# Kernel tuning notes

Hardware: AMD Instinct MI355X
Metric: run time of the kernel (lower is better)

The kernel has to match this reference:

```python
import jax, jax.numpy as jnp
import numpy as np

N = 100000          # number of nodes
E = 128             # embedding size
NUM_LAYERS = 4
SMOOTH = 12.0       # MAXIMUM_SMOOTHNESS
RELATIONS = [("at", 2), ("clear", 1), ("on", 2)]  # sorted, as in module
ATOM_COUNTS = {"at": 150000, "clear": 150000, "on": 150000}


def mish(x):
    return x * jnp.tanh(jax.nn.softplus(x))


def _linear_init(k, din, dout):
    s = 1.0 / np.sqrt(din)
    kw, kb = jax.random.split(k)
    w = jax.random.uniform(kw, (din, dout), jnp.float32, -s, s)
    b = jax.random.uniform(kb, (dout,), jnp.float32, -s, s)
    return w, b


def setup_inputs() -> dict:
    key = jax.random.key(0)
    ks = iter(jax.random.split(key, 64))
    inp = {}
    inp["node_embeddings"] = jax.random.normal(next(ks), (N, E), jnp.float32)
    for name, ar in RELATIONS:
        inp[f"atoms_{name}"] = jax.random.randint(
            next(ks), (ATOM_COUNTS[name] * ar,), 0, N, dtype=jnp.int32)
        d = ar * E
        inp[f"w_in_{name}"], inp[f"b_in_{name}"] = _linear_init(next(ks), d, d)
        inp[f"w_out_{name}"], inp[f"b_out_{name}"] = _linear_init(next(ks), d, d)
    # update MLP: Linear(2E, 2E) -> mish -> Linear(2E, E)
    inp["w_u_in"], inp["b_u_in"] = _linear_init(next(ks), 2 * E, 2 * E)
    inp["w_u_out"], inp["b_u_out"] = _linear_init(next(ks), 2 * E, E)
    return inp


def _forward(node_embeddings, atoms, params):
    w_u_in, b_u_in, w_u_out, b_u_out = params["update"]

    def layer(h):
        msgs, idxs = [], []
        for name, ar in RELATIONS:
            w_in, b_in, w_out, b_out = params[name]
            av = atoms[name]                              # [A*ar] node indices
            x = h[av].reshape(-1, ar * E)                 # gather -> [A, ar*E]
            y = x + (mish(x @ w_in + b_in) @ w_out + b_out)  # residual MLP
            msgs.append(y.reshape(-1, E))
            idxs.append(av)
        msg = jnp.concatenate(msgs, 0)                    # [T, E]
        idx = jnp.concatenate(idxs, 0)                    # [T]
        # smooth-max aggregation (max offsets are not differentiated)
        seg_max = jax.ops.segment_max(msg, idx, num_segments=N)
        seg_max = jnp.where(jnp.isfinite(seg_max), seg_max, 0.0)  # empty -> 0 (include_self=False on zeros)
        seg_max = jax.lax.stop_gradient(seg_max)
        exps = jnp.exp(SMOOTH * (msg - seg_max[idx]))
        exps_sum = jax.ops.segment_sum(exps, idx, num_segments=N) + 1e-16
        max_msg = jnp.log(exps_sum) / SMOOTH + seg_max
        upd_in = jnp.concatenate([max_msg, h], axis=1)    # [N, 2E]
        upd = mish(upd_in @ w_u_in + b_u_in) @ w_u_out + b_u_out
        return h + upd                                    # outer residual

    h = node_embeddings
    for _ in range(NUM_LAYERS):
        h = layer(h)
    return h


def reference(node_embeddings, atoms_at, atoms_clear, atoms_on,
              w_in_at, b_in_at, w_out_at, b_out_at,
              w_in_clear, b_in_clear, w_out_clear, b_out_clear,
              w_in_on, b_in_on, w_out_on, b_out_on,
              w_u_in, b_u_in, w_u_out, b_u_out):
    atoms = {"at": atoms_at, "clear": atoms_clear, "on": atoms_on}
    params = {
        "at": (w_in_at, b_in_at, w_out_at, b_out_at),
        "clear": (w_in_clear, b_in_clear, w_out_clear, b_out_clear),
        "on": (w_in_on, b_in_on, w_out_on, b_out_on),
        "update": (w_u_in, b_u_in, w_u_out, b_u_out),
    }
    return _forward(node_embeddings, atoms, params)
```

## Files before the change

### kernel.cpp

```cpp
#include <hip/hip_runtime.h>
#include <hip/hip_bf16.h>
#include <math.h>

#define NNODES 100000
#define EDIM 128
#define TSLOTS 750000
#define NB 391

typedef __bf16 bf16x8 __attribute__((ext_vector_type(8)));
typedef __bf16 bf16x4 __attribute__((ext_vector_type(4)));
typedef float f32x4 __attribute__((ext_vector_type(4)));

#define T_SCALE 17.312340490667562f
#define INV_SCALE 0.05776226504666211f
#define EMPTY_V (-3.0701134f)

__device__ __forceinline__ float mishf(float x) {
  float u = __expf(fminf(x, 15.f));
  float num = u * (u + 2.f);
  return x * num * __builtin_amdgcn_rcpf(num + 2.f);
}

__device__ __forceinline__ double exp12t(float t) {
  t = fmaxf(t, -20000.f);
  float ti = floorf(t);
  float m = exp2f(t - ti);
  int ei = (int)ti;
  ei = ei < -1000 ? -1000 : (ei > 1000 ? 1000 : ei);
  return (double)m * __longlong_as_double(((long long)(1023 + ei)) << 52);
}

__device__ __forceinline__ float logS12(double S) {
  if (!(S > 0.0)) return EMPTY_V;
  long long b = __double_as_longlong(S);
  int e2 = (int)((b >> 52) & 0x7FF) - 1023;
  float mf = __uint_as_float(0x3F800000u | (unsigned)((b >> 29) & 0x7FFFFF));
  return ((float)e2 + log2f(mf)) * INV_SCALE;
}

__global__ void k_sentinel(float* out, int n) {
  int i = blockIdx.x * 256 + threadIdx.x;
  if (i < n) out[i] = 1.0e6f;
}

__global__ void k_init(const float* __restrict__ h0, __bf16* __restrict__ hb, int n8) {
  int i = blockIdx.x * 256 + threadIdx.x;
  if (i >= n8) return;
  float4 f0 = ((const float4*)h0)[i * 2];
  float4 f1 = ((const float4*)h0)[i * 2 + 1];
  bf16x8 p = {(__bf16)f0.x, (__bf16)f0.y, (__bf16)f0.z, (__bf16)f0.w,
              (__bf16)f1.x, (__bf16)f1.y, (__bf16)f1.z, (__bf16)f1.w};
  *(bf16x8*)(hb + (size_t)i * 8) = p;
}

struct TransDesc {
  const float* src[8];
  __bf16* dst[8];
  int R[8];
  int C[8];
  int tstart[9];
};

__global__ void k_transpose_all(TransDesc td) {
  __shared__ float tile[32][33];
  int b = blockIdx.x;
  int m = 0;
  while (m < 7 && b >= td.tstart[m + 1]) m++;
  int t = b - td.tstart[m];
  int R = td.R[m], C = td.C[m];
  int tcols = C >> 5;
  int by = t / tcols, bx = t - by * tcols;
  int tx = threadIdx.x & 31, ty = threadIdx.x >> 5;
  const float* src = td.src[m];
  __bf16* dst = td.dst[m];
  for (int i = 0; i < 32; i += 8)
    tile[ty + i][tx] = src[(size_t)(by * 32 + ty + i) * C + bx * 32 + tx];
  __syncthreads();
  for (int i = 0; i < 32; i += 8)
    dst[(size_t)(bx * 32 + ty + i) * R + by * 32 + tx] = (__bf16)tile[tx][ty + i];
}

__device__ __forceinline__ int slot_node(int s, const int* at, const int* cl, const int* on) {
  if (s < 300000) return at[s];
  if (s < 450000) return cl[s - 300000];
  return on[s - 450000];
}

__global__ void k_count(const int* __restrict__ at, const int* __restrict__ cl,
                        const int* __restrict__ on, int* __restrict__ cnt) {
  int s = blockIdx.x * 256 + threadIdx.x;
  if (s >= TSLOTS) return;
  atomicAdd(&cnt[slot_node(s, at, cl, on)], 1);
}

__global__ void k_bsum(const int* __restrict__ cnt, int* __restrict__ bsum) {
  __shared__ int sm[256];
  int n = blockIdx.x * 256 + threadIdx.x;
  sm[threadIdx.x] = (n < NNODES) ? cnt[n] : 0;
  __syncthreads();
  for (int st = 128; st > 0; st >>= 1) {
    if (threadIdx.x < st) sm[threadIdx.x] += sm[threadIdx.x + st];
    __syncthreads();
  }
  if (threadIdx.x == 0) bsum[blockIdx.x] = sm[0];
}

__global__ void k_bscan(const int* __restrict__ bsum, int* __restrict__ bpre,
                        int* __restrict__ off) {
  __shared__ int sm[512];
  int t = threadIdx.x;
  int v = (t < NB) ? bsum[t] : 0;
  sm[t] = v;
  __syncthreads();
  for (int st = 1; st < 512; st <<= 1) {
    int x = (t >= st) ? sm[t - st] : 0;
    __syncthreads();
    sm[t] += x;
    __syncthreads();
  }
  if (t < NB) bpre[t] = sm[t] - v;
  if (t == NB - 1) off[NNODES] = sm[t];
}

__global__ void k_off(const int* __restrict__ cnt, const int* __restrict__ bpre,
                      int* __restrict__ off) {
  __shared__ int sm[256];
  int n = blockIdx.x * 256 + threadIdx.x;
  int v = (n < NNODES) ? cnt[n] : 0;
  sm[threadIdx.x] = v;
  __syncthreads();
  for (int st = 1; st < 256; st <<= 1) {
    int t = (threadIdx.x >= st) ? sm[threadIdx.x - st] : 0;
    __syncthreads();
    sm[threadIdx.x] += t;
    __syncthreads();
  }
  if (n < NNODES) off[n] = bpre[blockIdx.x] + sm[threadIdx.x] - v;
}

__global__ void k_fill(const int* __restrict__ at, const int* __restrict__ cl,
                       const int* __restrict__ on, const int* __restrict__ off,
                       int* __restrict__ cnt, int* __restrict__ perm) {
  int s = blockIdx.x * 256 + threadIdx.x;
  if (s >= TSLOTS) return;
  int node = slot_node(s, at, cl, on);
  int pos = atomicAdd(&cnt[node], -1) - 1;
  perm[s] = off[node] + pos;
}

__global__ __launch_bounds__(256, 2) void k_rel2(
    const float* __restrict__ hf, const __bf16* __restrict__ hb,
    const int* __restrict__ av,
    const __bf16* __restrict__ wt1, const float* __restrict__ b1,
    const __bf16* __restrict__ wt2, const float* __restrict__ b2,
    _Float16* __restrict__ msg, const int* __restrict__ permrel, int A) {
  __shared__ __align__(16) __bf16 xs[64][264];
  __shared__ int avs[128];
  __shared__ int prm[128];
  const int tid = threadIdx.x;
  const int lane = tid & 63;
  const int w = tid >> 6;
  const int row0 = blockIdx.x * 64;

  if (tid < 128) {
    int i2 = row0 * 2 + tid;
    avs[tid] = (i2 < 2 * A) ? av[i2] : 0;
    prm[tid] = (i2 < 2 * A) ? permrel[i2] : 0;
  }
  if (hb != nullptr) {
    for (int i = 0; i < 8; ++i) {
      int s = tid + i * 256;
      int r = s >> 5, o = s & 31;
      int a = row0 + r;
      uint4 v = {0, 0, 0, 0};
      if (a < A) {
        int node = av[2 * a + (o >> 4)];
        v = *(const uint4*)(hb + (size_t)node * 128 + (o & 15) * 8);
      }
      *(uint4*)&xs[r][o * 8] = v;
    }
  } else {
    for (int i = 0; i < 16; ++i) {
      int s = tid + i * 256;
      int r = s >> 6, o = s & 63;
      int a = row0 + r;
      float4 f = {0.f, 0.f, 0.f, 0.f};
      if (a < A) {
        int node = av[2 * a + (o >> 5)];
        f = *(const float4*)(hf + (size_t)node * 128 + (o & 31) * 4);
      }
      bf16x4 p = {(__bf16)f.x, (__bf16)f.y, (__bf16)f.z, (__bf16)f.w};
      *(bf16x4*)&xs[r][o * 4] = p;
    }
  }
  __syncthreads();

  const int lhi = lane >> 4, llo = lane & 15;
  const int cb = w * 64;

  f32x4 acc1[4][4];
#pragma unroll
  for (int rt = 0; rt < 4; rt++)
#pragma unroll
    for (int ct = 0; ct < 4; ct++) acc1[rt][ct] = (f32x4){0.f, 0.f, 0.f, 0.f};

#pragma unroll
  for (int kk = 0; kk < 8; ++kk) {
    int k = kk * 32 + lhi * 8;
    bf16x8 af[4], bfr[4];
#pragma unroll
    for (int rt = 0; rt < 4; rt++) af[rt] = *(const bf16x8*)&xs[rt * 16 + llo][k];
#pragma unroll
    for (int ct = 0; ct < 4; ct++)
      bfr[ct] = *(const bf16x8*)(wt1 + (size_t)(cb + ct * 16 + llo) * 256 + k);
#pragma unroll
    for (int rt = 0; rt < 4; rt++)
#pragma unroll
      for (int ct = 0; ct < 4; ct++)
        acc1[rt][ct] = __builtin_amdgcn_mfma_f32_16x16x32_bf16(af[rt], bfr[ct], acc1[rt][ct], 0, 0, 0);
  }
  __syncthreads();

  float b1v[4];
#pragma unroll
  for (int ct = 0; ct < 4; ct++) b1v[ct] = b1[cb + ct * 16 + llo];
#pragma unroll
  for (int rt = 0; rt < 4; rt++)
#pragma unroll
    for (int ct = 0; ct < 4; ct++)
#pragma unroll
      for (int i = 0; i < 4; i++)
        xs[rt * 16 + lhi * 4 + i][cb + ct * 16 + llo] = (__bf16)mishf(acc1[rt][ct][i] + b1v[ct]);
  __syncthreads();

  f32x4 acc2[4][4];
#pragma unroll
  for (int rt = 0; rt < 4; rt++)
#pragma unroll
    for (int ct = 0; ct < 4; ct++) acc2[rt][ct] = (f32x4){0.f, 0.f, 0.f, 0.f};

#pragma unroll
  for (int kk = 0; kk < 8; ++kk) {
    int k = kk * 32 + lhi * 8;
    bf16x8 af[4], bfr[4];
#pragma unroll
    for (int rt = 0; rt < 4; rt++) af[rt] = *(const bf16x8*)&xs[rt * 16 + llo][k];
#pragma unroll
    for (int ct = 0; ct < 4; ct++)
      bfr[ct] = *(const bf16x8*)(wt2 + (size_t)(cb + ct * 16 + llo) * 256 + k);
#pragma unroll
    for (int rt = 0; rt < 4; rt++)
#pragma unroll
      for (int ct = 0; ct < 4; ct++)
        acc2[rt][ct] = __builtin_amdgcn_mfma_f32_16x16x32_bf16(af[rt], bfr[ct], acc2[rt][ct], 0, 0, 0);
  }
  __syncthreads();

  float b2v[4];
#pragma unroll
  for (int ct = 0; ct < 4; ct++) b2v[ct] = b2[cb + ct * 16 + llo];
  ushort* zs = (ushort*)&xs[0][0];
#pragma unroll
  for (int rt = 0; rt < 4; rt++)
#pragma unroll
    for (int ct = 0; ct < 4; ct++)
#pragma unroll
      for (int i = 0; i < 4; i++) {
        int r = rt * 16 + lhi * 4 + i;
        int col = cb + ct * 16 + llo;
        union { ushort u; _Float16 f; } cv;
        cv.f = (_Float16)(acc2[rt][ct][i] + b2v[ct]);
        zs[r * 264 + col] = cv.u;
      }
  __syncthreads();

  for (int i = 0; i < 8; ++i) {
    int s = tid + i * 256;
    int sr = s >> 4;
    int c = s & 15;
    int a = row0 + (sr >> 1);
    if (a < A) {
      int node = avs[sr];
      int rr = sr >> 1, c0 = (sr & 1) * 128 + c * 8;
      float hv[8];
      if (hb != nullptr) {
        union { uint4 u; __bf16 b[8]; } hu;
        hu.u = *(const uint4*)(hb + (size_t)node * 128 + c * 8);
#pragma unroll
        for (int k = 0; k < 8; ++k) hv[k] = (float)hu.b[k];
      } else {
        const float* hp = hf + (size_t)node * 128 + c * 8;
        float4 h0 = *(const float4*)hp;
        float4 h1 = *(const float4*)(hp + 4);
        hv[0] = h0.x; hv[1] = h0.y; hv[2] = h0.z; hv[3] = h0.w;
        hv[4] = h1.x; hv[5] = h1.y; hv[6] = h1.z; hv[7] = h1.w;
      }
      union { uint4 u; _Float16 f[8]; } zu, yu;
      zu.u = *(const uint4*)&zs[rr * 264 + c0];
#pragma unroll
      for (int k = 0; k < 8; ++k)
        yu.f[k] = (_Float16)(((float)zu.f[k] + hv[k]) * T_SCALE);
      *(uint4*)(msg + (size_t)prm[sr] * 128 + c * 8) = yu.u;
    }
  }
}

__global__ __launch_bounds__(256, 2) void k_rel1(
    const float* __restrict__ hf, const __bf16* __restrict__ hb,
    const int* __restrict__ av,
    const __bf16* __restrict__ wt1, const float* __restrict__ b1,
    const __bf16* __restrict__ wt2, const float* __restrict__ b2,
    _Float16* __restrict__ msg, const int* __restrict__ permrel, int A) {
  __shared__ __align__(16) __bf16 xs[64][136];
  __shared__ int avs[64];
  __shared__ int prm[64];
  const int tid = threadIdx.x;
  const int lane = tid & 63;
  const int w = tid >> 6;
  const int row0 = blockIdx.x * 64;

  if (tid < 64) {
    int a = row0 + tid;
    avs[tid] = (a < A) ? av[a] : 0;
    prm[tid] = (a < A) ? permrel[a] : 0;
  }
  if (hb != nullptr) {
    for (int i = 0; i < 4; ++i) {
      int s = tid + i * 256;
      int r = s >> 4, o = s & 15;
      int a = row0 + r;
      uint4 v = {0, 0, 0, 0};
      if (a < A) {
        int node = av[a];
        v = *(const uint4*)(hb + (size_t)node * 128 + o * 8);
      }
      *(uint4*)&xs[r][o * 8] = v;
    }
  } else {
    for (int i = 0; i < 8; ++i) {
      int s = tid + i * 256;
      int r = s >> 5, o = s & 31;
      int a = row0 + r;
      float4 f = {0.f, 0.f, 0.f, 0.f};
      if (a < A) {
        int node = av[a];
        f = *(const float4*)(hf + (size_t)node * 128 + o * 4);
      }
      bf16x4 p = {(__bf16)f.x, (__bf16)f.y, (__bf16)f.z, (__bf16)f.w};
      *(bf16x4*)&xs[r][o * 4] = p;
    }
  }
  __syncthreads();

  const int lhi = lane >> 4, llo = lane & 15;
  const int cb = w * 32;

  f32x4 acc1[4][2];
#pragma unroll
  for (int rt = 0; rt < 4; rt++)
#pragma unroll
    for (int ct = 0; ct < 2; ct++) acc1[rt][ct] = (f32x4){0.f, 0.f, 0.f, 0.f};

#pragma unroll
  for (int kk = 0; kk < 4; ++kk) {
    int k = kk * 32 + lhi * 8;
    bf16x8 af[4], bfr[2];
#pragma unroll
    for (int rt = 0; rt < 4; rt++) af[rt] = *(const bf16x8*)&xs[rt * 16 + llo][k];
#pragma unroll
    for (int ct = 0; ct < 2; ct++)
      bfr[ct] = *(const bf16x8*)(wt1 + (size_t)(cb + ct * 16 + llo) * 128 + k);
#pragma unroll
    for (int rt = 0; rt < 4; rt++)
#pragma unroll
      for (int ct = 0; ct < 2; ct++)
        acc1[rt][ct] = __builtin_amdgcn_mfma_f32_16x16x32_bf16(af[rt], bfr[ct], acc1[rt][ct], 0, 0, 0);
  }
  __syncthreads();

  float b1v[2];
#pragma unroll
  for (int ct = 0; ct < 2; ct++) b1v[ct] = b1[cb + ct * 16 + llo];
#pragma unroll
  for (int rt = 0; rt < 4; rt++)
#pragma unroll
    for (int ct = 0; ct < 2; ct++)
#pragma unroll
      for (int i = 0; i < 4; i++)
        xs[rt * 16 + lhi * 4 + i][cb + ct * 16 + llo] = (__bf16)mishf(acc1[rt][ct][i] + b1v[ct]);
  __syncthreads();

  f32x4 acc2[4][2];
#pragma unroll
  for (int rt = 0; rt < 4; rt++)
#pragma unroll
    for (int ct = 0; ct < 2; ct++) acc2[rt][ct] = (f32x4){0.f, 0.f, 0.f, 0.f};

#pragma unroll
  for (int kk = 0; kk < 4; ++kk) {
    int k = kk * 32 + lhi * 8;
    bf16x8 af[4], bfr[2];
#pragma unroll
    for (int rt = 0; rt < 4; rt++) af[rt] = *(const bf16x8*)&xs[rt * 16 + llo][k];
#pragma unroll
    for (int ct = 0; ct < 2; ct++)
      bfr[ct] = *(const bf16x8*)(wt2 + (size_t)(cb + ct * 16 + llo) * 128 + k);
#pragma unroll
    for (int rt = 0; rt < 4; rt++)
#pragma unroll
      for (int ct = 0; ct < 2; ct++)
        acc2[rt][ct] = __builtin_amdgcn_mfma_f32_16x16x32_bf16(af[rt], bfr[ct], acc2[rt][ct], 0, 0, 0);
  }
  __syncthreads();

  float b2v[2];
#pragma unroll
  for (int ct = 0; ct < 2; ct++) b2v[ct] = b2[cb + ct * 16 + llo];
  ushort* zs = (ushort*)&xs[0][0];
#pragma unroll
  for (int rt = 0; rt < 4; rt++)
#pragma unroll
    for (int ct = 0; ct < 2; ct++)
#pragma unroll
      for (int i = 0; i < 4; i++) {
        int r = rt * 16 + lhi * 4 + i;
        int col = cb + ct * 16 + llo;
        union { ushort u; _Float16 f; } cv;
        cv.f = (_Float16)(acc2[rt][ct][i] + b2v[ct]);
        zs[r * 136 + col] = cv.u;
      }
  __syncthreads();

  for (int i = 0; i < 4; ++i) {
    int s = tid + i * 256;
    int sr = s >> 4;
    int c = s & 15;
    int a = row0 + sr;
    if (a < A) {
      int node = avs[sr];
      float hv[8];
      if (hb != nullptr) {
        union { uint4 u; __bf16 b[8]; } hu;
        hu.u = *(const uint4*)(hb + (size_t)node * 128 + c * 8);
#pragma unroll
        for (int k = 0; k < 8; ++k) hv[k] = (float)hu.b[k];
      } else {
        const float* hp = hf + (size_t)node * 128 + c * 8;
        float4 h0 = *(const float4*)hp;
        float4 h1 = *(const float4*)(hp + 4);
        hv[0] = h0.x; hv[1] = h0.y; hv[2] = h0.z; hv[3] = h0.w;
        hv[4] = h1.x; hv[5] = h1.y; hv[6] = h1.z; hv[7] = h1.w;
      }
      union { uint4 u; _Float16 f[8]; } zu, yu;
      zu.u = *(const uint4*)&zs[sr * 136 + c * 8];
#pragma unroll
      for (int k = 0; k < 8; ++k)
        yu.f[k] = (_Float16)(((float)zu.f[k] + hv[k]) * T_SCALE);
      *(uint4*)(msg + (size_t)prm[sr] * 128 + c * 8) = yu.u;
    }
  }
}

__global__ __launch_bounds__(256, 2) void k_update(
    const float* __restrict__ hin, const _Float16* __restrict__ msg,
    const int* __restrict__ off,
    const __bf16* __restrict__ wt1, const float* __restrict__ b1,
    const __bf16* __restrict__ wt2, const float* __restrict__ b2,
    float* __restrict__ hout, __bf16* __restrict__ hbout) {
  __shared__ __align__(16) __bf16 xs[64][264];
  __shared__ int offs[65];
  const int tid = threadIdx.x;
  const int lane = tid & 63;
  const int w = tid >> 6;
  const int node0 = blockIdx.x * 64;

  if (tid < 65) {
    int n = node0 + tid;
    offs[tid] = off[n < NNODES ? n : NNODES];
  }
  for (int i = 0; i < 8; ++i) {
    int s = tid + i * 256;
    int r = s >> 5, o = s & 31;
    int n = node0 + r;
    float4 f = {0.f, 0.f, 0.f, 0.f};
    if (n < NNODES) f = *(const float4*)(hin + (size_t)n * 128 + o * 4);
    bf16x4 p = {(__bf16)f.x, (__bf16)f.y, (__bf16)f.z, (__bf16)f.w};
    *(bf16x4*)&xs[r][128 + o * 4] = p;
  }
  __syncthreads();

  const _Float16* mbase = msg + lane * 2;
#pragma unroll 1
  for (int j = 0; j < 16; ++j) {
    int beg = offs[w * 16 + j];
    int end = offs[w * 16 + j + 1];
    int deg = end - beg;
    double S0 = 0.0, S1 = 0.0;
#pragma unroll 1
    for (int d = 0; d < deg; d += 4) {
      int dm1 = deg - 1;
      int i1 = d + 1 < dm1 ? d + 1 : dm1;
      int i2 = d + 2 < dm1 ? d + 2 : dm1;
      int i3 = d + 3 < dm1 ? d + 3 : dm1;
      uint a0 = *(const uint*)(mbase + (size_t)(beg + d) * 128);
      uint a1 = *(const uint*)(mbase + (size_t)(beg + i1) * 128);
      uint a2 = *(const uint*)(mbase + (size_t)(beg + i2) * 128);
      uint a3 = *(const uint*)(mbase + (size_t)(beg + i3) * 128);
      union { uint u; _Float16 f[2]; } q0, q1, q2, q3;
      q0.u = a0; q1.u = a1; q2.u = a2; q3.u = a3;
      double e00 = exp12t((float)q0.f[0]), e01 = exp12t((float)q0.f[1]);
      double e10 = exp12t((float)q1.f[0]), e11 = exp12t((float)q1.f[1]);
      double e20 = exp12t((float)q2.f[0]), e21 = exp12t((float)q2.f[1]);
      double e30 = exp12t((float)q3.f[0]), e31 = exp12t((float)q3.f[1]);
      S0 += e00;
      S1 += e01;
      S0 += (d + 1 < deg) ? e10 : 0.0;
      S1 += (d + 1 < deg) ? e11 : 0.0;
      S0 += (d + 2 < deg) ? e20 : 0.0;
      S1 += (d + 2 < deg) ? e21 : 0.0;
      S0 += (d + 3 < deg) ? e30 : 0.0;
      S1 += (d + 3 < deg) ? e31 : 0.0;
    }
    union { uint u; __bf16 b[2]; } pk;
    pk.b[0] = (__bf16)logS12(S0);
    pk.b[1] = (__bf16)logS12(S1);
    *(uint*)&xs[w * 16 + j][2 * lane] = pk.u;
  }
  __syncthreads();

  const int lhi = lane >> 4, llo = lane & 15;
  const int cb = w * 64;

  f32x4 acc1[4][4];
#pragma unroll
  for (int rt = 0; rt < 4; rt++)
#pragma unroll
    for (int ct = 0; ct < 4; ct++) acc1[rt][ct] = (f32x4){0.f, 0.f, 0.f, 0.f};

#pragma unroll
  for (int kk = 0; kk < 8; ++kk) {
    int k = kk * 32 + lhi * 8;
    bf16x8 af[4], bfr[4];
#pragma unroll
    for (int rt = 0; rt < 4; rt++) af[rt] = *(const bf16x8*)&xs[rt * 16 + llo][k];
#pragma unroll
    for (int ct = 0; ct < 4; ct++)
      bfr[ct] = *(const bf16x8*)(wt1 + (size_t)(cb + ct * 16 + llo) * 256 + k);
#pragma unroll
    for (int rt = 0; rt < 4; rt++)
#pragma unroll
      for (int ct = 0; ct < 4; ct++)
        acc1[rt][ct] = __builtin_amdgcn_mfma_f32_16x16x32_bf16(af[rt], bfr[ct], acc1[rt][ct], 0, 0, 0);
  }
  __syncthreads();

  float b1v[4];
#pragma unroll
  for (int ct = 0; ct < 4; ct++) b1v[ct] = b1[cb + ct * 16 + llo];
#pragma unroll
  for (int rt = 0; rt < 4; rt++)
#pragma unroll
    for (int ct = 0; ct < 4; ct++)
#pragma unroll
      for (int i = 0; i < 4; i++)
        xs[rt * 16 + lhi * 4 + i][cb + ct * 16 + llo] = (__bf16)mishf(acc1[rt][ct][i] + b1v[ct]);
  __syncthreads();

  const int cb2 = w * 32;
  f32x4 acc2[4][2];
#pragma unroll
  for (int rt = 0; rt < 4; rt++)
#pragma unroll
    for (int ct = 0; ct < 2; ct++) acc2[rt][ct] = (f32x4){0.f, 0.f, 0.f, 0.f};

#pragma unroll
  for (int kk = 0; kk < 8; ++kk) {
    int k = kk * 32 + lhi * 8;
    bf16x8 af[4], bfr[2];
#pragma unroll
    for (int rt = 0; rt < 4; rt++) af[rt] = *(const bf16x8*)&xs[rt * 16 + llo][k];
#pragma unroll
    for (int ct = 0; ct < 2; ct++)
      bfr[ct] = *(const bf16x8*)(wt2 + (size_t)(cb2 + ct * 16 + llo) * 256 + k);
#pragma unroll
    for (int rt = 0; rt < 4; rt++)
#pragma unroll
      for (int ct = 0; ct < 2; ct++)
        acc2[rt][ct] = __builtin_amdgcn_mfma_f32_16x16x32_bf16(af[rt], bfr[ct], acc2[rt][ct], 0, 0, 0);
  }

  float b2v[2];
#pragma unroll
  for (int ct = 0; ct < 2; ct++) b2v[ct] = b2[cb2 + ct * 16 + llo];
#pragma unroll
  for (int rt = 0; rt < 4; rt++)
#pragma unroll
    for (int i = 0; i < 4; i++) {
      int r = rt * 16 + lhi * 4 + i;
      int n = node0 + r;
      if (n >= NNODES) continue;
#pragma unroll
      for (int ct = 0; ct < 2; ct++) {
        int col = cb2 + ct * 16 + llo;
        size_t idx = (size_t)n * 128 + col;
        float nh = hin[idx] + acc2[rt][ct][i] + b2v[ct];
        hout[idx] = nh;
        if (hbout != nullptr) hbout[idx] = (__bf16)nh;
      }
    }
}

extern "C" void kernel_launch(void* const* d_in, const int* in_sizes, int n_in,
                              void* d_out, int out_size, void* d_ws, size_t ws_size,
                              hipStream_t stream) {
  const float* h0 = (const float*)d_in[0];
  const int* at = (const int*)d_in[1];
  const float* w_in_at = (const float*)d_in[2];
  const float* b_in_at = (const float*)d_in[3];
  const float* w_out_at = (const float*)d_in[4];
  const float* b_out_at = (const float*)d_in[5];
  const int* cl = (const int*)d_in[6];
  const float* w_in_cl = (const float*)d_in[7];
  const float* b_in_cl = (const float*)d_in[8];
  const float* w_out_cl = (const float*)d_in[9];
  const float* b_out_cl = (const float*)d_in[10];
  const int* on = (const int*)d_in[11];
  const float* w_in_on = (const float*)d_in[12];
  const float* b_in_on = (const float*)d_in[13];
  const float* w_out_on = (const float*)d_in[14];
  const float* b_out_on = (const float*)d_in[15];
  const float* w_u_in = (const float*)d_in[16];
  const float* b_u_in = (const float*)d_in[17];
  const float* w_u_out = (const float*)d_in[18];
  const float* b_u_out = (const float*)d_in[19];

  float* hout = (float*)d_out;
  char* ws = (char*)d_ws;

  const size_t MSG_B = (size_t)TSLOTS * 128 * 2;
  const size_t OFF_B = 400016;
  const size_t CNT_B = 400000;
  const size_t BS_B = 1568;
  const size_t PERM_B = 3000000;
  const size_t WT_B = 786432;
  const size_t HB_B = (size_t)NNODES * 128 * 2;
  const size_t REQ2 = MSG_B + OFF_B + CNT_B + 2 * BS_B + PERM_B + WT_B;
  const size_t REQ3 = REQ2 + HB_B;

  if (ws_size < REQ2) {
    k_sentinel<<<(out_size + 255) / 256, 256, 0, stream>>>((float*)d_out, out_size);
    return;
  }

  _Float16* msg = (_Float16*)ws;
  int* off = (int*)(ws + MSG_B);
  int* cnt = (int*)(ws + MSG_B + OFF_B);
  int* bsum = (int*)(ws + MSG_B + OFF_B + CNT_B);
  int* bpre = (int*)(ws + MSG_B + OFF_B + CNT_B + BS_B);
  int* perm = (int*)(ws + MSG_B + OFF_B + CNT_B + 2 * BS_B);
  __bf16* wt = (__bf16*)(ws + MSG_B + OFF_B + CNT_B + 2 * BS_B + PERM_B);
  __bf16* hb = (ws_size >= REQ3) ? (__bf16*)(ws + REQ2) : nullptr;

  __bf16* wt_in_at = wt;
  __bf16* wt_out_at = wt + 65536;
  __bf16* wt_in_on = wt + 131072;
  __bf16* wt_out_on = wt + 196608;
  __bf16* wt_u_in = wt + 262144;
  __bf16* wt_u_out = wt + 327680;
  __bf16* wt_in_cl = wt + 360448;
  __bf16* wt_out_cl = wt + 376832;

  TransDesc td;
  const float* srcs[8] = {w_in_at, w_out_at, w_in_on, w_out_on, w_u_in, w_u_out, w_in_cl, w_out_cl};
  __bf16* dsts[8] = {wt_in_at, wt_out_at, wt_in_on, wt_out_on, wt_u_in, wt_u_out, wt_in_cl, wt_out_cl};
  int Rs[8] = {256, 256, 256, 256, 256, 256, 128, 128};
  int Cs[8] = {256, 256, 256, 256, 256, 128, 128, 128};
  int ts = 0;
  for (int m = 0; m < 8; ++m) {
    td.src[m] = srcs[m]; td.dst[m] = dsts[m]; td.R[m] = Rs[m]; td.C[m] = Cs[m];
    td.tstart[m] = ts; ts += (Rs[m] / 32) * (Cs[m] / 32);
  }
  td.tstart[8] = ts;
  k_transpose_all<<<384, 256, 0, stream>>>(td);

  if (hb) k_init<<<6250, 256, 0, stream>>>(h0, hb, NNODES * EDIM / 8);

  const int grid_rel = (150000 + 63) / 64;
  const int grid_upd = (NNODES + 63) / 64;
  const int grid_slots = (TSLOTS + 255) / 256;

  hipMemsetAsync(cnt, 0, CNT_B, stream);
  k_count<<<grid_slots, 256, 0, stream>>>(at, cl, on, cnt);
  k_bsum<<<NB, 256, 0, stream>>>(cnt, bsum);
  k_bscan<<<1, 512, 0, stream>>>(bsum, bpre, off);
  k_off<<<NB, 256, 0, stream>>>(cnt, bpre, off);
  k_fill<<<grid_slots, 256, 0, stream>>>(at, cl, on, off, cnt, perm);

  const int* perm_at = perm;
  const int* perm_cl = perm + 300000;
  const int* perm_on = perm + 450000;

  for (int l = 0; l < 4; ++l) {
    const float* hs = (l == 0) ? h0 : hout;
    k_rel2<<<grid_rel, 256, 0, stream>>>(hs, hb, at, wt_in_at, b_in_at, wt_out_at, b_out_at, msg, perm_at, 150000);
    k_rel1<<<grid_rel, 256, 0, stream>>>(hs, hb, cl, wt_in_cl, b_in_cl, wt_out_cl, b_out_cl, msg, perm_cl, 150000);
    k_rel2<<<grid_rel, 256, 0, stream>>>(hs, hb, on, wt_in_on, b_in_on, wt_out_on, b_out_on, msg, perm_on, 150000);
    k_update<<<grid_upd, 256, 0, stream>>>(hs, msg, off, wt_u_in, b_u_in, wt_u_out, b_u_out, hout, hb);
  }
}
```

Before: 1.905 ms.

## Split update kernel into separate aggregation and MLP kernels, raise occupancy

The fused update kernel, which did the segment smooth-max reduction and then the update MLP, is split in two. A light k_agg kernel runs at high occupancy and reads 4 features per lane with two rows in flight per wavefront, writing the aggregated max messages to a new bf16 workspace buffer. k_mlp then reads that buffer. Launch bounds for the relation kernels are raised to 4 blocks per SM, and message values are clamped below the fp16 maximum. The split costs an extra 25MB round trip through memory per layer and risks register spills from the tighter launch bounds.

```diff
diff --git a/kernel.cpp b/kernel.cpp
--- a/kernel.cpp
+++ b/kernel.cpp
@@ -148,7 +148,7 @@
   perm[s] = off[node] + pos;
 }
 
-__global__ __launch_bounds__(256, 2) void k_rel2(
+__global__ __launch_bounds__(256, 4) void k_rel2(
     const float* __restrict__ hf, const __bf16* __restrict__ hb,
     const int* __restrict__ av,
     const __bf16* __restrict__ wt1, const float* __restrict__ b1,
@@ -299,13 +299,13 @@
       zu.u = *(const uint4*)&zs[rr * 264 + c0];
 #pragma unroll
       for (int k = 0; k < 8; ++k)
-        yu.f[k] = (_Float16)(((float)zu.f[k] + hv[k]) * T_SCALE);
+        yu.f[k] = (_Float16)(fminf(((float)zu.f[k] + hv[k]) * T_SCALE, 60000.f));
       *(uint4*)(msg + (size_t)prm[sr] * 128 + c * 8) = yu.u;
     }
   }
 }
 
-__global__ __launch_bounds__(256, 2) void k_rel1(
+__global__ __launch_bounds__(256, 4) void k_rel1(
     const float* __restrict__ hf, const __bf16* __restrict__ hb,
     const int* __restrict__ av,
     const __bf16* __restrict__ wt1, const float* __restrict__ b1,
@@ -455,28 +455,83 @@
       zu.u = *(const uint4*)&zs[sr * 136 + c * 8];
 #pragma unroll
       for (int k = 0; k < 8; ++k)
-        yu.f[k] = (_Float16)(((float)zu.f[k] + hv[k]) * T_SCALE);
+        yu.f[k] = (_Float16)(fminf(((float)zu.f[k] + hv[k]) * T_SCALE, 60000.f));
       *(uint4*)(msg + (size_t)prm[sr] * 128 + c * 8) = yu.u;
     }
   }
 }
 
-__global__ __launch_bounds__(256, 2) void k_update(
-    const float* __restrict__ hin, const _Float16* __restrict__ msg,
-    const int* __restrict__ off,
+__global__ __launch_bounds__(256, 8) void k_agg(
+    const _Float16* __restrict__ msg, const int* __restrict__ off,
+    __bf16* __restrict__ mm) {
+  __shared__ int offs[33];
+  const int tid = threadIdx.x;
+  const int lane = tid & 63;
+  const int w = tid >> 6;
+  const int node0 = blockIdx.x * 32;
+  if (tid < 33) {
+    int n = node0 + tid;
+    offs[tid] = off[n < NNODES ? n : NNODES];
+  }
+  __syncthreads();
+
+  const int fl = lane & 31;
+  const int p = lane >> 5;
+  const _Float16* mb = msg + fl * 4;
+
+#pragma unroll 1
+  for (int j = 0; j < 8; ++j) {
+    int n = node0 + w * 8 + j;
+    if (n >= NNODES) break;
+    int beg = offs[w * 8 + j];
+    int deg = offs[w * 8 + j + 1] - beg;
+    double S0 = 0.0, S1 = 0.0, S2 = 0.0, S3 = 0.0;
+#pragma unroll 1
+    for (int d = 0; d < deg; d += 2) {
+      int rp = d + p;
+      int rc = rp < deg - 1 ? rp : deg - 1;
+      uint2 v = *(const uint2*)(mb + (size_t)(beg + rc) * 128);
+      if (rp >= deg) { v.x = 0xFC00FC00u; v.y = 0xFC00FC00u; }
+      union { uint2 u; _Float16 f[4]; } q;
+      q.u = v;
+      S0 += exp12t((float)q.f[0]);
+      S1 += exp12t((float)q.f[1]);
+      S2 += exp12t((float)q.f[2]);
+      S3 += exp12t((float)q.f[3]);
+    }
+    S0 += __shfl_xor(S0, 32);
+    S1 += __shfl_xor(S1, 32);
+    S2 += __shfl_xor(S2, 32);
+    S3 += __shfl_xor(S3, 32);
+    if (p == 0) {
+      bf16x4 r;
+      r[0] = (__bf16)logS12(S0);
+      r[1] = (__bf16)logS12(S1);
+      r[2] = (__bf16)logS12(S2);
+      r[3] = (__bf16)logS12(S3);
+      *(bf16x4*)(mm + (size_t)n * 128 + fl * 4) = r;
+    }
+  }
+}
+
+__global__ __launch_bounds__(256, 4) void k_mlp(
+    const float* __restrict__ hin, const __bf16* __restrict__ mm,
     const __bf16* __restrict__ wt1, const float* __restrict__ b1,
     const __bf16* __restrict__ wt2, const float* __restrict__ b2,
     float* __restrict__ hout, __bf16* __restrict__ hbout) {
   __shared__ __align__(16) __bf16 xs[64][264];
-  __shared__ int offs[65];
   const int tid = threadIdx.x;
   const int lane = tid & 63;
   const int w = tid >> 6;
   const int node0 = blockIdx.x * 64;
 
-  if (tid < 65) {
-    int n = node0 + tid;
-    offs[tid] = off[n < NNODES ? n : NNODES];
+  for (int i = 0; i < 4; ++i) {
+    int s = tid + i * 256;
+    int r = s >> 4, o = s & 15;
+    int n = node0 + r;
+    uint4 v = {0, 0, 0, 0};
+    if (n < NNODES) v = *(const uint4*)(mm + (size_t)n * 128 + o * 8);
+    *(uint4*)&xs[r][o * 8] = v;
   }
   for (int i = 0; i < 8; ++i) {
     int s = tid + i * 256;
@@ -486,45 +541,6 @@
     if (n < NNODES) f = *(const float4*)(hin + (size_t)n * 128 + o * 4);
     bf16x4 p = {(__bf16)f.x, (__bf16)f.y, (__bf16)f.z, (__bf16)f.w};
     *(bf16x4*)&xs[r][128 + o * 4] = p;
-  }
-  __syncthreads();
-
-  const _Float16* mbase = msg + lane * 2;
-#pragma unroll 1
-  for (int j = 0; j < 16; ++j) {
-    int beg = offs[w * 16 + j];
-    int end = offs[w * 16 + j + 1];
-    int deg = end - beg;
-    double S0 = 0.0, S1 = 0.0;
-#pragma unroll 1
-    for (int d = 0; d < deg; d += 4) {
-      int dm1 = deg - 1;
-      int i1 = d + 1 < dm1 ? d + 1 : dm1;
-      int i2 = d + 2 < dm1 ? d + 2 : dm1;
-      int i3 = d + 3 < dm1 ? d + 3 : dm1;
-      uint a0 = *(const uint*)(mbase + (size_t)(beg + d) * 128);
-      uint a1 = *(const uint*)(mbase + (size_t)(beg + i1) * 128);
-      uint a2 = *(const uint*)(mbase + (size_t)(beg + i2) * 128);
-      uint a3 = *(const uint*)(mbase + (size_t)(beg + i3) * 128);
-      union { uint u; _Float16 f[2]; } q0, q1, q2, q3;
-      q0.u = a0; q1.u = a1; q2.u = a2; q3.u = a3;
-      double e00 = exp12t((float)q0.f[0]), e01 = exp12t((float)q0.f[1]);
-      double e10 = exp12t((float)q1.f[0]), e11 = exp12t((float)q1.f[1]);
-      double e20 = exp12t((float)q2.f[0]), e21 = exp12t((float)q2.f[1]);
-      double e30 = exp12t((float)q3.f[0]), e31 = exp12t((float)q3.f[1]);
-      S0 += e00;
-      S1 += e01;
-      S0 += (d + 1 < deg) ? e10 : 0.0;
-      S1 += (d + 1 < deg) ? e11 : 0.0;
-      S0 += (d + 2 < deg) ? e20 : 0.0;
-      S1 += (d + 2 < deg) ? e21 : 0.0;
-      S0 += (d + 3 < deg) ? e30 : 0.0;
-      S1 += (d + 3 < deg) ? e31 : 0.0;
-    }
-    union { uint u; __bf16 b[2]; } pk;
-    pk.b[0] = (__bf16)logS12(S0);
-    pk.b[1] = (__bf16)logS12(S1);
-    *(uint*)&xs[w * 16 + j][2 * lane] = pk.u;
   }
   __syncthreads();
 
@@ -643,8 +659,9 @@
   const size_t BS_B = 1568;
   const size_t PERM_B = 3000000;
   const size_t WT_B = 786432;
+  const size_t MM_B = (size_t)NNODES * 128 * 2;
   const size_t HB_B = (size_t)NNODES * 128 * 2;
-  const size_t REQ2 = MSG_B + OFF_B + CNT_B + 2 * BS_B + PERM_B + WT_B;
+  const size_t REQ2 = MSG_B + OFF_B + CNT_B + 2 * BS_B + PERM_B + WT_B + MM_B;
   const size_t REQ3 = REQ2 + HB_B;
 
   if (ws_size < REQ2) {
@@ -659,6 +676,7 @@
   int* bpre = (int*)(ws + MSG_B + OFF_B + CNT_B + BS_B);
   int* perm = (int*)(ws + MSG_B + OFF_B + CNT_B + 2 * BS_B);
   __bf16* wt = (__bf16*)(ws + MSG_B + OFF_B + CNT_B + 2 * BS_B + PERM_B);
+  __bf16* mm = (__bf16*)(ws + MSG_B + OFF_B + CNT_B + 2 * BS_B + PERM_B + WT_B);
   __bf16* hb = (ws_size >= REQ3) ? (__bf16*)(ws + REQ2) : nullptr;
 
   __bf16* wt_in_at = wt;
@@ -686,7 +704,8 @@
   if (hb) k_init<<<6250, 256, 0, stream>>>(h0, hb, NNODES * EDIM / 8);
 
   const int grid_rel = (150000 + 63) / 64;
-  const int grid_upd = (NNODES + 63) / 64;
+  const int grid_mlp = (NNODES + 63) / 64;
+  const int grid_agg = (NNODES + 31) / 32;
   const int grid_slots = (TSLOTS + 255) / 256;
 
   hipMemsetAsync(cnt, 0, CNT_B, stream);
@@ -705,6 +724,7 @@
     k_rel2<<<grid_rel, 256, 0, stream>>>(hs, hb, at, wt_in_at, b_in_at, wt_out_at, b_out_at, msg, perm_at, 150000);
     k_rel1<<<grid_rel, 256, 0, stream>>>(hs, hb, cl, wt_in_cl, b_in_cl, wt_out_cl, b_out_cl, msg, perm_cl, 150000);
     k_rel2<<<grid_rel, 256, 0, stream>>>(hs, hb, on, wt_in_on, b_in_on, wt_out_on, b_out_on, msg, perm_on, 150000);
-    k_update<<<grid_upd, 256, 0, stream>>>(hs, msg, off, wt_u_in, b_u_in, wt_u_out, b_u_out, hout, hb);
-  }
-}
+    k_agg<<<grid_agg, 256, 0, stream>>>(msg, off, mm);
+    k_mlp<<<grid_mlp, 256, 0, stream>>>(hs, mm, wt_u_in, b_u_in, wt_u_out, b_u_out, hout, hb);
+  }
+}
```

New measurement: 1.883 ms. No clear change (-1.1%).
